# Kernel optimization log

Measured on AMD Instinct MI355X. Metric: run time of the kernel, lower is better.

Reference implementation:

```python
import jax, jax.numpy as jnp
import numpy as np


def setup_inputs() -> dict:
    key = jax.random.key(0)
    k0, k1, k2, k3 = jax.random.split(key, 4)
    B, T, C = 4, 2048, 1024
    x = jax.random.normal(k0, (B, T, C), dtype=jnp.float32)
    s = C ** -0.5  # init-scale for weights so activations stay O(1)
    Wq = jax.random.normal(k1, (C, C), dtype=jnp.float32) * s
    Wk = jax.random.normal(k2, (C, C), dtype=jnp.float32) * s
    Wv = jax.random.normal(k3, (C, C), dtype=jnp.float32) * s
    return {"x": x, "Wq": Wq, "Wk": Wk, "Wv": Wv}


def reference(x, Wq, Wk, Wv):
    B, T, C = x.shape
    # torch nn.Linear: y = x @ W.T
    q = jnp.einsum('btc,dc->btd', x, Wq)
    k = jnp.einsum('btc,dc->btd', x, Wk)
    v = jnp.einsum('btc,dc->btd', x, Wv)
    scale = C ** -0.5
    wei = jnp.einsum('btd,bsd->bts', q, k) * scale  # [B, T, T]
    causal = jnp.tril(jnp.ones((T, T), dtype=bool))
    wei = jnp.where(causal, wei, -jnp.inf)
    wei = jax.nn.softmax(wei, axis=-1)
    out = jnp.einsum('bts,bsd->btd', wei, v)
    return out
```

## Files before the change

### kernel.cpp

```cpp
#include <hip/hip_runtime.h>
#include <hip/hip_bf16.h>
#include <math.h>

#define B_ 4
#define T_ 2048
#define C_ 1024
#define M_ (B_*T_)

typedef __attribute__((ext_vector_type(8))) __bf16 bf16x8;
typedef __attribute__((ext_vector_type(4))) float floatx4;

__device__ inline float bf2f(unsigned short u){
    return __uint_as_float(((unsigned)u) << 16);
}
__device__ inline unsigned short f2bf(float f){
    unsigned u = __float_as_uint(f);
    unsigned r = (u + 0x7fffu + ((u >> 16) & 1u)) >> 16;
    return (unsigned short)r;
}

__device__ inline void llds16(const unsigned short* g, unsigned short* lds){
    __builtin_amdgcn_global_load_lds(
        (const __attribute__((address_space(1))) unsigned int*)g,
        (__attribute__((address_space(3))) unsigned int*)(unsigned int)(uintptr_t)lds,
        16, 0, 0);
}

#define NX_ (M_*C_/4)
#define NW_ (C_*C_/4)
__global__ __launch_bounds__(256) void cast_all(
    const float* __restrict__ x, const float* __restrict__ wq,
    const float* __restrict__ wk, const float* __restrict__ wv,
    unsigned short* __restrict__ xb, unsigned short* __restrict__ wb)
{
    int i = blockIdx.x * 256 + threadIdx.x;
    const float* src; unsigned short* dst; int idx;
    if (i < NX_){ src = x; dst = xb; idx = i; }
    else {
        i -= NX_;
        int w = i / NW_; idx = i - w * NW_;
        src = (w == 0) ? wq : ((w == 1) ? wk : wv);
        dst = wb + (size_t)w * C_ * C_;
    }
    float4 v = ((const float4*)src)[idx];
    ((ushort4*)dst)[idx] = make_ushort4(f2bf(v.x), f2bf(v.y), f2bf(v.z), f2bf(v.w));
}

template<int WM, int WN>
__device__ inline void gemm_core(const unsigned short* __restrict__ A,
                                 const unsigned short* __restrict__ Bm,
                                 int lda, int ldb, int m0, int n0, int kTiles,
                                 unsigned short* As, unsigned short* Bs,
                                 floatx4 (*acc)[WN/16])
{
    const int tid  = threadIdx.x;
    const int lane = tid & 63;
    const int wave = tid >> 6;
    const int wm = (wave >> 1) * WM;
    const int wn = (wave & 1) * WN;
    const int fr = lane & 15;
    const int fq = lane >> 4;
    const int cxor = fr & 7;
    const int sr = lane >> 3;
    const int sc = ((lane & 7) ^ ((lane >> 3) & 7)) * 8;

    const unsigned short* gA = A  + (size_t)(m0 + wave * (WM/2) + sr) * lda + sc;
    const unsigned short* gB = Bm + (size_t)(n0 + wave * (WN/2) + sr) * ldb + sc;
    unsigned short* ldsA = As + wave * (WM/2) * 64;
    unsigned short* ldsB = Bs + wave * (WN/2) * 64;

    for (int kt = 0; kt < kTiles; kt++){
        const int k0 = kt * 64;
        __syncthreads();
        #pragma unroll
        for (int i = 0; i < WM/16; i++)
            llds16(gA + (size_t)(i * 8) * lda + k0, ldsA + i * 8 * 64);
        #pragma unroll
        for (int i = 0; i < WN/16; i++)
            llds16(gB + (size_t)(i * 8) * ldb + k0, ldsB + i * 8 * 64);
        __syncthreads();
        #pragma unroll
        for (int ks = 0; ks < 64; ks += 32){
            const int cpos = (((ks >> 3) + fq) ^ cxor) * 8;
            bf16x8 af[WM/16], bv[WN/16];
            #pragma unroll
            for (int i = 0; i < WM/16; i++)
                af[i] = *(const bf16x8*)(As + (wm + i*16 + fr) * 64 + cpos);
            #pragma unroll
            for (int j = 0; j < WN/16; j++)
                bv[j] = *(const bf16x8*)(Bs + (wn + j*16 + fr) * 64 + cpos);
            #pragma unroll
            for (int i = 0; i < WM/16; i++)
                #pragma unroll
                for (int j = 0; j < WN/16; j++)
                    acc[i][j] = __builtin_amdgcn_mfma_f32_16x16x32_bf16(af[i], bv[j], acc[i][j], 0, 0, 0);
        }
    }
}

__global__ __launch_bounds__(256, 4) void proj_gemm(
    const unsigned short* __restrict__ xb,
    const unsigned short* __restrict__ Wb,
    unsigned short* __restrict__ Qb, unsigned short* __restrict__ Kb,
    unsigned short* __restrict__ Vt)
{
    __shared__ unsigned short As[128 * 64];
    __shared__ unsigned short Bs[128 * 64];
    const int L = blockIdx.x;
    const int k = L & 7, j = L >> 3;
    const int m0 = (k * 8 + (j & 7)) * 128;
    const int n0 = ((j >> 3) & 7) * 128;
    const int z  = j >> 6;
    const unsigned short* W = Wb + (size_t)z * C_ * C_;

    floatx4 acc[4][4];
    #pragma unroll
    for (int i = 0; i < 4; i++)
        #pragma unroll
        for (int jj = 0; jj < 4; jj++) acc[i][jj] = (floatx4){0.f,0.f,0.f,0.f};
    gemm_core<64, 64>(xb, W, C_, C_, m0, n0, C_ / 64, As, Bs, acc);

    const int lane = threadIdx.x & 63, wave = threadIdx.x >> 6;
    const int wm = (wave >> 1) * 64, wn = (wave & 1) * 64;
    const int fr = lane & 15, fq = lane >> 4;

    if (z < 2){
        unsigned short* Y = z ? Kb : Qb;
        #pragma unroll
        for (int i = 0; i < 4; i++)
            #pragma unroll
            for (int jj = 0; jj < 4; jj++)
                #pragma unroll
                for (int r = 0; r < 4; r++){
                    int row = m0 + wm + i*16 + fq*4 + r;
                    int col = n0 + wn + jj*16 + fr;
                    Y[(size_t)row * C_ + col] = f2bf(acc[i][jj][r]);
                }
    } else {
        #pragma unroll
        for (int i = 0; i < 4; i++)
            #pragma unroll
            for (int jj = 0; jj < 4; jj++){
                int row = m0 + wm + i*16 + fq*4;
                int col = n0 + wn + jj*16 + fr;
                int b = row / T_, t = row % T_;
                ushort4 o = make_ushort4(f2bf(acc[i][jj][0]), f2bf(acc[i][jj][1]),
                                         f2bf(acc[i][jj][2]), f2bf(acc[i][jj][3]));
                *(ushort4*)&Vt[(size_t)b * C_ * T_ + (size_t)col * T_ + t] = o;
            }
    }
}

__global__ __launch_bounds__(256, 4) void score_gemm(
    const unsigned short* __restrict__ Qb, const unsigned short* __restrict__ Kb,
    unsigned short* __restrict__ P, float* __restrict__ l)
{
    const int L = blockIdx.x;
    const int k = L & 7, j = L >> 3;
    const int b = j / 34, rem = j % 34;
    const int th = rem & 1, rr = rem >> 1;
    int ti, si;
    if (rr <= 15 - k){ ti = 15 - k; si = rr; }
    else             { ti = k;      si = rr - (16 - k); }
    const int t0 = ti * 128 + th * 64, s0 = si * 128;

    __shared__ unsigned short As[64 * 64];
    __shared__ unsigned short Bs[128 * 64];
    floatx4 acc[2][4];
    #pragma unroll
    for (int i = 0; i < 2; i++)
        #pragma unroll
        for (int jj = 0; jj < 4; jj++) acc[i][jj] = (floatx4){0.f,0.f,0.f,0.f};
    gemm_core<32, 64>(Qb + (size_t)b * T_ * C_, Kb + (size_t)b * T_ * C_,
                      C_, C_, t0, s0, C_ / 64, As, Bs, acc);

    const int lane = threadIdx.x & 63, wave = threadIdx.x >> 6;
    const int wm = (wave >> 1) * 32, wn = (wave & 1) * 64;
    const int fr = lane & 15, fq = lane >> 4;
    unsigned short* Pb = P + (size_t)b * T_ * T_;
    const float scale = 0.03125f;
    float rsl[2][4];
    #pragma unroll
    for (int i = 0; i < 2; i++)
        #pragma unroll
        for (int r2 = 0; r2 < 4; r2++) rsl[i][r2] = 0.f;

    #pragma unroll
    for (int i = 0; i < 2; i++)
        #pragma unroll
        for (int jj = 0; jj < 4; jj++)
            #pragma unroll
            for (int r2 = 0; r2 < 4; r2++){
                int t = t0 + wm + i*16 + fq*4 + r2;
                int s = s0 + wn + jj*16 + fr;
                float v = (s <= t) ? __expf(acc[i][jj][r2] * scale) : 0.f;
                rsl[i][r2] += v;
                Pb[(size_t)t * T_ + s] = f2bf(v);
            }
    #pragma unroll
    for (int i = 0; i < 2; i++)
        #pragma unroll
        for (int r2 = 0; r2 < 4; r2++){
            float v = rsl[i][r2];
            v += __shfl_xor(v, 1, 64);
            v += __shfl_xor(v, 2, 64);
            v += __shfl_xor(v, 4, 64);
            v += __shfl_xor(v, 8, 64);
            if (fr == 0){
                int t = t0 + wm + i*16 + fq*4 + r2;
                atomicAdd(&l[(size_t)b * T_ + t], v);
            }
        }
}

__global__ __launch_bounds__(256, 4) void pv_gemm(
    const unsigned short* __restrict__ P, const unsigned short* __restrict__ Vt,
    const float* __restrict__ l, float* __restrict__ out)
{
    const int L = blockIdx.x;
    const int k = L & 7, j = L >> 3;
    const int b = j >> 4;
    const int n0 = (j & 15) * 64;

    __shared__ unsigned short As[128 * 64];
    __shared__ unsigned short Bs[64 * 64];

    const int lane = threadIdx.x & 63, wave = threadIdx.x >> 6;
    const int wm = (wave >> 1) * 64, wn = (wave & 1) * 32;
    const int fr = lane & 15, fq = lane >> 4;
    float* ob = out + (size_t)b * T_ * C_;
    const float* lb = l + (size_t)b * T_;

    #pragma unroll
    for (int phase = 0; phase < 2; phase++){
        const int ti = phase ? k : (15 - k);
        const int t0 = ti * 128;
        const int kTiles = 2 * (ti + 1);

        floatx4 acc[4][2];
        #pragma unroll
        for (int i = 0; i < 4; i++)
            #pragma unroll
            for (int jj = 0; jj < 2; jj++) acc[i][jj] = (floatx4){0.f,0.f,0.f,0.f};
        gemm_core<64, 32>(P + (size_t)b * T_ * T_, Vt + (size_t)b * C_ * T_,
                          T_, T_, t0, n0, kTiles, As, Bs, acc);

        #pragma unroll
        for (int i = 0; i < 4; i++){
            float inv[4];
            #pragma unroll
            for (int r2 = 0; r2 < 4; r2++)
                inv[r2] = 1.f / lb[t0 + wm + i*16 + fq*4 + r2];
            #pragma unroll
            for (int jj = 0; jj < 2; jj++)
                #pragma unroll
                for (int r2 = 0; r2 < 4; r2++){
                    int t = t0 + wm + i*16 + fq*4 + r2;
                    int d = n0 + wn + jj*16 + fr;
                    ob[(size_t)t * C_ + d] = acc[i][jj][r2] * inv[r2];
                }
        }
    }
}

extern "C" void kernel_launch(void* const* d_in, const int* in_sizes, int n_in,
                              void* d_out, int out_size, void* d_ws, size_t ws_size,
                              hipStream_t stream)
{
    const float* x  = (const float*)d_in[0];
    const float* Wq = (const float*)d_in[1];
    const float* Wk = (const float*)d_in[2];
    const float* Wv = (const float*)d_in[3];
    float* out = (float*)d_out;

    unsigned short* Qb = (unsigned short*)d_ws;
    unsigned short* Kb = Qb + (size_t)M_ * C_;
    unsigned short* Vt = Kb + (size_t)M_ * C_;
    unsigned short* P  = Vt + (size_t)M_ * C_;
    float* l = (float*)(P + (size_t)M_ * T_);
    unsigned short* xb = P;
    unsigned short* Wb = P + (size_t)M_ * C_;

    cast_all<<<(NX_ + 3 * NW_ + 255) / 256, 256, 0, stream>>>(x, Wq, Wk, Wv, xb, Wb);
    hipMemsetAsync(l, 0, (size_t)M_ * sizeof(float), stream);
    proj_gemm <<<1536, 256, 0, stream>>>(xb, Wb, Qb, Kb, Vt);
    score_gemm<<<1088, 256, 0, stream>>>(Qb, Kb, P, l);
    pv_gemm   <<<512,  256, 0, stream>>>(P, Vt, l, out);
}
```

Baseline: 215.5 us.

## Fuse fp32-to-bf16 cast of x into projection GEMM tile loads

The projection GEMM now reads fp32 x directly. Each thread converts its values to bf16 in registers and writes them into LDS in the same swizzled layout that global_load_lds used. This removes the separate cast pass over x and the bf16 copy of x in the workspace. The zeroing of the row-sum buffer moves into the weight-cast kernel, replacing the separate memset. In exchange, the projection kernel reads twice as many bytes for A on every k-tile and goes through registers instead of the direct global-to-LDS path, which may add latency inside the main loop.

Measured after the change: 250.4 us. 16.2% more time.

```diff
diff --git a/kernel.cpp b/kernel.cpp
--- a/kernel.cpp
+++ b/kernel.cpp
@@ -10,14 +10,11 @@
 typedef __attribute__((ext_vector_type(8))) __bf16 bf16x8;
 typedef __attribute__((ext_vector_type(4))) float floatx4;
 
-__device__ inline float bf2f(unsigned short u){
-    return __uint_as_float(((unsigned)u) << 16);
-}
-__device__ inline unsigned short f2bf(float f){
+__device__ inline unsigned f2bf_u(float f){
     unsigned u = __float_as_uint(f);
-    unsigned r = (u + 0x7fffu + ((u >> 16) & 1u)) >> 16;
-    return (unsigned short)r;
-}
+    return (u + 0x7fffu + ((u >> 16) & 1u)) >> 16;
+}
+__device__ inline unsigned short f2bf(float f){ return (unsigned short)f2bf_u(f); }
 
 __device__ inline void llds16(const unsigned short* g, unsigned short* lds){
     __builtin_amdgcn_global_load_lds(
@@ -26,28 +23,25 @@
         16, 0, 0);
 }
 
-#define NX_ (M_*C_/4)
 #define NW_ (C_*C_/4)
-__global__ __launch_bounds__(256) void cast_all(
-    const float* __restrict__ x, const float* __restrict__ wq,
-    const float* __restrict__ wk, const float* __restrict__ wv,
-    unsigned short* __restrict__ xb, unsigned short* __restrict__ wb)
+__global__ __launch_bounds__(256) void cast_w(
+    const float* __restrict__ wq, const float* __restrict__ wk,
+    const float* __restrict__ wv, unsigned short* __restrict__ wb,
+    float* __restrict__ l)
 {
     int i = blockIdx.x * 256 + threadIdx.x;
-    const float* src; unsigned short* dst; int idx;
-    if (i < NX_){ src = x; dst = xb; idx = i; }
-    else {
-        i -= NX_;
-        int w = i / NW_; idx = i - w * NW_;
-        src = (w == 0) ? wq : ((w == 1) ? wk : wv);
-        dst = wb + (size_t)w * C_ * C_;
-    }
+    if (i < M_) l[i] = 0.f;
+    if (i >= 3 * NW_) return;
+    int w = i / NW_;
+    int idx = i - w * NW_;
+    const float* src = (w == 0) ? wq : ((w == 1) ? wk : wv);
     float4 v = ((const float4*)src)[idx];
-    ((ushort4*)dst)[idx] = make_ushort4(f2bf(v.x), f2bf(v.y), f2bf(v.z), f2bf(v.w));
-}
-
-template<int WM, int WN>
-__device__ inline void gemm_core(const unsigned short* __restrict__ A,
+    ((ushort4*)(wb + (size_t)w * C_ * C_))[idx] =
+        make_ushort4(f2bf(v.x), f2bf(v.y), f2bf(v.z), f2bf(v.w));
+}
+
+template<int WM, int WN, bool AF32>
+__device__ inline void gemm_core(const void* __restrict__ Aptr,
                                  const unsigned short* __restrict__ Bm,
                                  int lda, int ldb, int m0, int n0, int kTiles,
                                  unsigned short* As, unsigned short* Bs,
@@ -64,7 +58,10 @@
     const int sr = lane >> 3;
     const int sc = ((lane & 7) ^ ((lane >> 3) & 7)) * 8;
 
-    const unsigned short* gA = A  + (size_t)(m0 + wave * (WM/2) + sr) * lda + sc;
+    const unsigned short* gA16 = nullptr;
+    const float*          gA32 = nullptr;
+    if (AF32) gA32 = (const float*)Aptr + (size_t)(m0 + wave * (WM/2) + sr) * lda + sc;
+    else      gA16 = (const unsigned short*)Aptr + (size_t)(m0 + wave * (WM/2) + sr) * lda + sc;
     const unsigned short* gB = Bm + (size_t)(n0 + wave * (WN/2) + sr) * ldb + sc;
     unsigned short* ldsA = As + wave * (WM/2) * 64;
     unsigned short* ldsB = Bs + wave * (WN/2) * 64;
@@ -72,9 +69,24 @@
     for (int kt = 0; kt < kTiles; kt++){
         const int k0 = kt * 64;
         __syncthreads();
-        #pragma unroll
-        for (int i = 0; i < WM/16; i++)
-            llds16(gA + (size_t)(i * 8) * lda + k0, ldsA + i * 8 * 64);
+        if (AF32){
+            #pragma unroll
+            for (int i = 0; i < WM/16; i++){
+                const float* p = gA32 + (size_t)(i * 8) * lda + k0;
+                float4 f0 = *(const float4*)p;
+                float4 f1 = *(const float4*)(p + 4);
+                uint4 o;
+                o.x = f2bf_u(f0.x) | (f2bf_u(f0.y) << 16);
+                o.y = f2bf_u(f0.z) | (f2bf_u(f0.w) << 16);
+                o.z = f2bf_u(f1.x) | (f2bf_u(f1.y) << 16);
+                o.w = f2bf_u(f1.z) | (f2bf_u(f1.w) << 16);
+                *(uint4*)(ldsA + i * 8 * 64 + lane * 8) = o;
+            }
+        } else {
+            #pragma unroll
+            for (int i = 0; i < WM/16; i++)
+                llds16(gA16 + (size_t)(i * 8) * lda + k0, ldsA + i * 8 * 64);
+        }
         #pragma unroll
         for (int i = 0; i < WN/16; i++)
             llds16(gB + (size_t)(i * 8) * ldb + k0, ldsB + i * 8 * 64);
@@ -99,7 +111,7 @@
 }
 
 __global__ __launch_bounds__(256, 4) void proj_gemm(
-    const unsigned short* __restrict__ xb,
+    const float* __restrict__ x,
     const unsigned short* __restrict__ Wb,
     unsigned short* __restrict__ Qb, unsigned short* __restrict__ Kb,
     unsigned short* __restrict__ Vt)
@@ -118,7 +130,7 @@
     for (int i = 0; i < 4; i++)
         #pragma unroll
         for (int jj = 0; jj < 4; jj++) acc[i][jj] = (floatx4){0.f,0.f,0.f,0.f};
-    gemm_core<64, 64>(xb, W, C_, C_, m0, n0, C_ / 64, As, Bs, acc);
+    gemm_core<64, 64, true>(x, W, C_, C_, m0, n0, C_ / 64, As, Bs, acc);
 
     const int lane = threadIdx.x & 63, wave = threadIdx.x >> 6;
     const int wm = (wave >> 1) * 64, wn = (wave & 1) * 64;
@@ -171,8 +183,8 @@
     for (int i = 0; i < 2; i++)
         #pragma unroll
         for (int jj = 0; jj < 4; jj++) acc[i][jj] = (floatx4){0.f,0.f,0.f,0.f};
-    gemm_core<32, 64>(Qb + (size_t)b * T_ * C_, Kb + (size_t)b * T_ * C_,
-                      C_, C_, t0, s0, C_ / 64, As, Bs, acc);
+    gemm_core<32, 64, false>(Qb + (size_t)b * T_ * C_, Kb + (size_t)b * T_ * C_,
+                             C_, C_, t0, s0, C_ / 64, As, Bs, acc);
 
     const int lane = threadIdx.x & 63, wave = threadIdx.x >> 6;
     const int wm = (wave >> 1) * 32, wn = (wave & 1) * 64;
@@ -242,8 +254,8 @@
         for (int i = 0; i < 4; i++)
             #pragma unroll
             for (int jj = 0; jj < 2; jj++) acc[i][jj] = (floatx4){0.f,0.f,0.f,0.f};
-        gemm_core<64, 32>(P + (size_t)b * T_ * T_, Vt + (size_t)b * C_ * T_,
-                          T_, T_, t0, n0, kTiles, As, Bs, acc);
+        gemm_core<64, 32, false>(P + (size_t)b * T_ * T_, Vt + (size_t)b * C_ * T_,
+                                 T_, T_, t0, n0, kTiles, As, Bs, acc);
 
         #pragma unroll
         for (int i = 0; i < 4; i++){
@@ -278,12 +290,10 @@
     unsigned short* Vt = Kb + (size_t)M_ * C_;
     unsigned short* P  = Vt + (size_t)M_ * C_;
     float* l = (float*)(P + (size_t)M_ * T_);
-    unsigned short* xb = P;
-    unsigned short* Wb = P + (size_t)M_ * C_;
-
-    cast_all<<<(NX_ + 3 * NW_ + 255) / 256, 256, 0, stream>>>(x, Wq, Wk, Wv, xb, Wb);
-    hipMemsetAsync(l, 0, (size_t)M_ * sizeof(float), stream);
-    proj_gemm <<<1536, 256, 0, stream>>>(xb, Wb, Qb, Kb, Vt);
+    unsigned short* Wb = P;
+
+    cast_w    <<<(3 * NW_ + 255) / 256, 256, 0, stream>>>(Wq, Wk, Wv, Wb, l);
+    proj_gemm <<<1536, 256, 0, stream>>>(x, Wb, Qb, Kb, Vt);
     score_gemm<<<1088, 256, 0, stream>>>(Qb, Kb, P, l);
     pv_gemm   <<<512,  256, 0, stream>>>(P, Vt, l, out);
 }
```
